# Kernel tuning notes

Hardware: AMD Instinct MI355X
Metric: run time of the kernel (lower is better)

## Reference

```python
import jax, jax.numpy as jnp
import numpy as np

B, N, D = 16, 2048, 1024
H, DH = 8, 64
I = H * DH            # 512
L = 64                # num_latents
DEPTH = 6
FF = 4 * D


def setup_inputs() -> dict:
    key = jax.random.key(0)
    ks = jax.random.split(key, 8)
    s = 0.02  # weight scale to keep activations well-conditioned
    return {
        "x": jax.random.normal(ks[0], (B, N, D), jnp.float32),
        "mask": jax.random.randint(ks[1], (B, N), 0, 2, jnp.int32),
        "latents": jax.random.normal(ks[2], (L, D), jnp.float32),
        "ln_m_w": jnp.ones((DEPTH, D), jnp.float32),
        "ln_m_b": jnp.zeros((DEPTH, D), jnp.float32),
        "ln_l_w": jnp.ones((DEPTH, D), jnp.float32),
        "ln_l_b": jnp.zeros((DEPTH, D), jnp.float32),
        "Wq": jax.random.normal(ks[3], (DEPTH, D, I), jnp.float32) * s,
        "Wkv": jax.random.normal(ks[4], (DEPTH, D, 2 * I), jnp.float32) * s,
        "Wo": jax.random.normal(ks[5], (DEPTH, I, D), jnp.float32) * s,
        "ff_ln_w": jnp.ones((DEPTH, D), jnp.float32),
        "ff_ln_b": jnp.zeros((DEPTH, D), jnp.float32),
        "W1": jax.random.normal(ks[6], (DEPTH, D, FF), jnp.float32) * s,
        "W2": jax.random.normal(ks[7], (DEPTH, FF, D), jnp.float32) * s,
        "norm_w": jnp.ones((D,), jnp.float32),
        "norm_b": jnp.zeros((D,), jnp.float32),
    }


def _ln(x, w, b, eps=1e-5):
    mu = x.mean(-1, keepdims=True)
    var = ((x - mu) ** 2).mean(-1, keepdims=True)
    return (x - mu) * jax.lax.rsqrt(var + eps) * w + b


def reference(x, mask, latents, ln_m_w, ln_m_b, ln_l_w, ln_l_b,
              Wq, Wkv, Wo, ff_ln_w, ff_ln_b, W1, W2, norm_w, norm_b):
    b, n, d = x.shape
    Lq = latents.shape[0]
    depth = Wq.shape[0]
    h = H
    dh = Wq.shape[-1] // h
    scale = dh ** -0.5

    x4 = x[:, None]  # b 1 n d  (t = 1 media frame)
    lat = jnp.broadcast_to(latents, (b, 1, Lq, d)).astype(x.dtype)
    # mask==1 means masked-out; latents (L zeros) are always attendable
    fmask = jnp.concatenate([mask, jnp.zeros((b, Lq), mask.dtype)], axis=-1)
    mbool = (fmask == 1)[:, None, None, None, :]  # b 1 1 1 S -> broadcast to b t h i S

    for i in range(depth):
        xn = _ln(x4, ln_m_w[i], ln_m_b[i])
        lnl = _ln(lat, ln_l_w[i], ln_l_b[i])
        q = (lnl @ Wq[i]).reshape(b, 1, Lq, h, dh)
        kv = jnp.concatenate([xn, lnl], axis=-2) @ Wkv[i]  # b 1 S 2I
        k, v = jnp.split(kv, 2, axis=-1)
        S = k.shape[-2]
        k = k.reshape(b, 1, S, h, dh)
        v = v.reshape(b, 1, S, h, dh)
        sim = jnp.einsum('btihd,btjhd->bthij', q, k) * scale
        sim = jnp.where(mbool, -jnp.inf, sim)
        sim = sim - jax.lax.stop_gradient(sim.max(axis=-1, keepdims=True))
        attn = jax.nn.softmax(sim, axis=-1)
        out = jnp.einsum('bthij,btjhd->btihd', attn, v).reshape(b, 1, Lq, h * dh)
        lat = out @ Wo[i] + lat
        hf = jax.nn.gelu(_ln(lat, ff_ln_w[i], ff_ln_b[i]) @ W1[i], approximate=False)
        lat = hf @ W2[i] + lat
    return _ln(lat, norm_w, norm_b)
```

## Files before the change

kernel.cpp:

```cpp
#include <hip/hip_runtime.h>

typedef unsigned short u16;
typedef unsigned int u32;
typedef __attribute__((ext_vector_type(8))) short short8;
typedef __attribute__((ext_vector_type(4))) float f4;

#define DEV static __device__ __forceinline__

constexpr int BB = 16, NN = 2048, DD = 1024, HH = 8, DHD = 64, II = 512, LL = 64, DEPTHC = 6, FFC = 4096;

DEV u16 f2bf(float f) {
  union { float f; u32 u; } v; v.f = f;
  u32 r = v.u + 0x7FFFu + ((v.u >> 16) & 1u);
  return (u16)(r >> 16);
}

DEV u32 pack2(float lo, float hi) {
  return (u32)f2bf(lo) | ((u32)f2bf(hi) << 16);
}

typedef const u32 __attribute__((address_space(1)))* gas_p;
typedef u32 __attribute__((address_space(3)))* las_p;
DEV void gl_lds16(const void* g, void* l) {
  __builtin_amdgcn_global_load_lds((gas_p)g, (las_p)l, 16, 0, 0);
}

__global__ __launch_bounds__(256) void maskscan_k(const int* __restrict__ mask,
    int* __restrict__ idx, int* __restrict__ cnt) {
  int b = blockIdx.x, tid = threadIdx.x;
  int lane = tid & 63, wv = tid >> 6;
  const int* mrow = mask + (size_t)b * NN;
  int base = tid * 8;
  int keep[8]; int local = 0;
  #pragma unroll
  for (int j = 0; j < 8; j++) { keep[j] = (mrow[base + j] == 0); local += keep[j]; }
  int incl = local;
  #pragma unroll
  for (int off = 1; off < 64; off <<= 1) {
    int v = __shfl_up(incl, off, 64);
    if (lane >= off) incl += v;
  }
  __shared__ int wsum[4];
  if (lane == 63) wsum[wv] = incl;
  __syncthreads();
  int wbase = 0;
  for (int w = 0; w < wv; w++) wbase += wsum[w];
  int pos = wbase + incl - local;
  #pragma unroll
  for (int j = 0; j < 8; j++) if (keep[j]) idx[(size_t)b * NN + pos++] = base + j;
  if (tid == 255) cnt[b] = wbase + incl;
}

__global__ void zero_k(float* __restrict__ p, int n) {
  int i = blockIdx.x * 256 + threadIdx.x;
  if (i < n) p[i] = 0.f;
}

__global__ __launch_bounds__(256) void transp_w_k(const float* __restrict__ Wa, u16* __restrict__ WTa,
    int R, int C, int ctLog) {
  __shared__ float t[64][65];
  int gid = blockIdx.x;
  int depth = gid >> 10;
  int l = gid & 1023;
  int c0 = (l & ((1 << ctLog) - 1)) << 6;
  int r0 = (l >> ctLog) << 6;
  const float* in = Wa + (size_t)depth * 4096 * 1024;
  u16* o1 = WTa + (size_t)depth * 4096 * 1024;
  int tid = threadIdx.x;
  int lr = tid >> 4, lc4 = (tid & 15) * 4;
  #pragma unroll
  for (int p = 0; p < 4; p++) {
    int row = p * 16 + lr;
    float4 v = *(const float4*)&in[(size_t)(r0 + row) * C + c0 + lc4];
    t[row][lc4] = v.x; t[row][lc4+1] = v.y; t[row][lc4+2] = v.z; t[row][lc4+3] = v.w;
  }
  __syncthreads();
  int oc = tid >> 3;
  int rg = tid & 7;
  #pragma unroll
  for (int p = 0; p < 2; p++) {
    int c = p * 32 + oc;
    float v[8];
    #pragma unroll
    for (int k = 0; k < 8; k++) v[k] = t[rg * 8 + k][c];
    int4 o;
    o.x = (int)pack2(v[0], v[1]); o.y = (int)pack2(v[2], v[3]);
    o.z = (int)pack2(v[4], v[5]); o.w = (int)pack2(v[6], v[7]);
    *(int4*)&o1[(size_t)(c0 + c) * R + r0 + rg * 8] = o;
  }
}

__global__ __launch_bounds__(256) void qkvo_fused_k(
    const float* __restrict__ WqA, const float* __restrict__ WkvA, const float* __restrict__ WoA,
    const float* __restrict__ lnwA, const float* __restrict__ lnbA,
    u16* __restrict__ WqkvTA, u16* __restrict__ WoTA, u16* __restrict__ WkvTfA,
    float* __restrict__ biaskvA,
    const float* __restrict__ x, const int* __restrict__ idx, const int* __restrict__ cnt,
    u16* __restrict__ xcomp, const float* __restrict__ latents, float* __restrict__ lat) {
  __shared__ float t[64][65];
  __shared__ float red8[8];
  int gid = blockIdx.x;
  int tid = threadIdx.x;
  if (gid < 3072) {
    int depth = gid >> 9;
    int id = gid & 511;
    const float* in; u16* o1; int R, C, c0, r0;
    bool iskv = false;
    if (id < 128)      { in = WqA  + (size_t)depth*1024*512;  R = 1024; C = 512;  int l = id;       c0 = (l & 7) * 64;  r0 = (l >> 3) * 64; o1 = WqkvTA + (size_t)depth*1536*1024; }
    else if (id < 384) { in = WkvA + (size_t)depth*1024*1024; R = 1024; C = 1024; int l = id - 128; c0 = (l & 15) * 64; r0 = (l >> 4) * 64; o1 = WqkvTA + (size_t)depth*1536*1024 + 512*1024; iskv = true; }
    else               { in = WoA  + (size_t)depth*512*1024;  R = 512;  C = 1024; int l = id - 384; c0 = (l & 15) * 64; r0 = (l >> 4) * 64; o1 = WoTA + (size_t)depth*1024*512; }
    int lr = tid >> 4, lc4 = (tid & 15) * 4;
    #pragma unroll
    for (int p = 0; p < 4; p++) {
      int row = p * 16 + lr;
      float4 v = *(const float4*)&in[(size_t)(r0 + row) * C + c0 + lc4];
      t[row][lc4] = v.x; t[row][lc4+1] = v.y; t[row][lc4+2] = v.z; t[row][lc4+3] = v.w;
    }
    int oc = tid >> 3;
    int rg = tid & 7;
    float lw[8], lb[8];
    if (iskv) {
      const float* lnw = lnwA + depth * 1024;
      const float* lnb = lnbA + depth * 1024;
      int rbase = r0 + rg * 8;
      float4 w0 = *(const float4*)&lnw[rbase];
      float4 w1 = *(const float4*)&lnw[rbase + 4];
      float4 b0 = *(const float4*)&lnb[rbase];
      float4 b1 = *(const float4*)&lnb[rbase + 4];
      lw[0]=w0.x; lw[1]=w0.y; lw[2]=w0.z; lw[3]=w0.w; lw[4]=w1.x; lw[5]=w1.y; lw[6]=w1.z; lw[7]=w1.w;
      lb[0]=b0.x; lb[1]=b0.y; lb[2]=b0.z; lb[3]=b0.w; lb[4]=b1.x; lb[5]=b1.y; lb[6]=b1.z; lb[7]=b1.w;
    }
    __syncthreads();
    #pragma unroll
    for (int p = 0; p < 2; p++) {
      int c = p * 32 + oc;
      float v[8];
      #pragma unroll
      for (int k = 0; k < 8; k++) v[k] = t[rg * 8 + k][c];
      int4 o;
      o.x = (int)pack2(v[0], v[1]); o.y = (int)pack2(v[2], v[3]);
      o.z = (int)pack2(v[4], v[5]); o.w = (int)pack2(v[6], v[7]);
      *(int4*)&o1[(size_t)(c0 + c) * R + r0 + rg * 8] = o;
      if (iskv) {
        u16* WkvTf = WkvTfA + (size_t)depth*1024*1024;
        int4 of;
        of.x = (int)pack2(v[0]*lw[0], v[1]*lw[1]); of.y = (int)pack2(v[2]*lw[2], v[3]*lw[3]);
        of.z = (int)pack2(v[4]*lw[4], v[5]*lw[5]); of.w = (int)pack2(v[6]*lw[6], v[7]*lw[7]);
        *(int4*)&WkvTf[(size_t)(c0 + c) * 1024 + r0 + rg * 8] = of;
        float partial = 0.f;
        #pragma unroll
        for (int k = 0; k < 8; k++) partial += lb[k] * v[k];
        partial += __shfl_xor(partial, 1, 64);
        partial += __shfl_xor(partial, 2, 64);
        partial += __shfl_xor(partial, 4, 64);
        if (rg == 0) atomicAdd(&biaskvA[depth*1024 + c0 + c], partial);
      }
    }
    return;
  }
  gid -= 3072;
  if (gid < 32768) {
    int b = gid >> 11, j = gid & 2047;
    int c = cnt[b];
    if (j >= ((c + 127) & ~127)) return;
    ushort4* orow = (ushort4*)(xcomp + ((size_t)b * NN + j) * DD);
    if (j >= c) { orow[tid] = make_ushort4(0, 0, 0, 0); return; }
    int src = idx[(size_t)b * NN + j];
    const float4* rp = (const float4*)(x + ((size_t)b * NN + src) * DD);
    float4 v = rp[tid];
    float s = v.x + v.y + v.z + v.w;
    float s2 = v.x*v.x + v.y*v.y + v.z*v.z + v.w*v.w;
    #pragma unroll
    for (int off = 32; off >= 1; off >>= 1) {
      s  += __shfl_xor(s, off, 64);
      s2 += __shfl_xor(s2, off, 64);
    }
    int wv = tid >> 6;
    if ((tid & 63) == 0) { red8[wv] = s; red8[4 + wv] = s2; }
    __syncthreads();
    s  = red8[0] + red8[1] + red8[2] + red8[3];
    s2 = red8[4] + red8[5] + red8[6] + red8[7];
    float mu = s * (1.f / DD);
    float var = s2 * (1.f / DD) - mu * mu;
    float rstd = rsqrtf(var + 1e-5f);
    orow[tid] = make_ushort4(f2bf((v.x - mu) * rstd), f2bf((v.y - mu) * rstd),
                             f2bf((v.z - mu) * rstd), f2bf((v.w - mu) * rstd));
    return;
  }
  gid -= 32768;
  int i2 = gid * 256 + tid;
  ((float4*)lat)[i2] = ((const float4*)latents)[i2 & (LL * DD / 4 - 1)];
}

template<bool OUTF32>
__global__ __launch_bounds__(256) void ln_rows_k(const float* __restrict__ in,
    const float* __restrict__ w, const float* __restrict__ bias, void* __restrict__ out) {
  int row = blockIdx.x;
  int tid = threadIdx.x;
  const float4* rp = (const float4*)(in + (size_t)row * DD);
  float4 x = rp[tid];
  float s = x.x + x.y + x.z + x.w;
  float s2 = x.x*x.x + x.y*x.y + x.z*x.z + x.w*x.w;
  #pragma unroll
  for (int off = 32; off >= 1; off >>= 1) {
    s  += __shfl_xor(s, off, 64);
    s2 += __shfl_xor(s2, off, 64);
  }
  __shared__ float red[8];
  int wv = tid >> 6;
  if ((tid & 63) == 0) { red[wv] = s; red[4 + wv] = s2; }
  __syncthreads();
  s  = red[0] + red[1] + red[2] + red[3];
  s2 = red[4] + red[5] + red[6] + red[7];
  float mu = s * (1.f / DD);
  float var = s2 * (1.f / DD) - mu * mu;
  float rstd = rsqrtf(var + 1e-5f);
  float y[4] = {x.x, x.y, x.z, x.w};
  int col = tid * 4;
  #pragma unroll
  for (int j = 0; j < 4; j++)
    y[j] = (y[j] - mu) * rstd * w[col + j] + bias[col + j];
  if (OUTF32) {
    float4 o = {y[0], y[1], y[2], y[3]};
    ((float4*)out)[(size_t)row * (DD/4) + tid] = o;
  } else {
    ushort4 o = make_ushort4(f2bf(y[0]), f2bf(y[1]), f2bf(y[2]), f2bf(y[3]));
    ((ushort4*)out)[(size_t)row * (DD/4) + tid] = o;
  }
}

__global__ __launch_bounds__(256) void gemm_fused_k(
    const u16* __restrict__ xcomp, const u16* __restrict__ WkvTf,
    u16* __restrict__ kvk, u16* __restrict__ vT,
    const float* __restrict__ bias, const int* __restrict__ cnt,
    const u16* __restrict__ lnl, const u16* __restrict__ WqkvT, u16* __restrict__ qkv) {
  __shared__ __align__(16) u16 As[128 * 32];
  __shared__ __align__(16) u16 Bs[128 * 32];
  int id = blockIdx.x;
  int tid = threadIdx.x;
  int wv = tid >> 6, lane = tid & 63;
  const u16 *A, *B;
  int m0, n0, batch = 0, ml = 0;
  bool iskv;
  if (id < 2048) {
    int xg = id & 7, t = id >> 3;
    int mtile = xg * 32 + (t >> 3);
    n0 = (t & 7) * 128;
    batch = mtile >> 4;
    ml = (mtile & 15) * 128;
    if (ml >= cnt[batch]) return;
    m0 = batch * NN + ml;
    A = xcomp; B = WkvTf; iskv = true;
  } else {
    int l = id - 2048;
    m0 = (l / 12) * 128; n0 = (l % 12) * 128;
    A = lnl; B = WqkvT; iskv = false;
  }
  const int K = 1024;
  int srow = wv * 16 + (lane >> 2);
  int scol = (lane & 3) * 8;
  const u16* gA0 = A + (size_t)(m0 + srow) * K + scol;
  const u16* gA1 = A + (size_t)(m0 + 64 + srow) * K + scol;
  const u16* gB0 = B + (size_t)(n0 + srow) * K + scol;
  const u16* gB1 = B + (size_t)(n0 + 64 + srow) * K + scol;
  u16* lA0 = &As[srow * 32 + scol];
  u16* lA1 = &As[(64 + srow) * 32 + scol];
  u16* lB0 = &Bs[srow * 32 + scol];
  u16* lB1 = &Bs[(64 + srow) * 32 + scol];
  int wm = (wv & 1) * 64, wn = (wv >> 1) * 64;
  int fr = lane & 15, fq = (lane >> 4) * 8;
  f4 acc[4][4];
  #pragma unroll
  for (int mi = 0; mi < 4; mi++)
    #pragma unroll
    for (int ni = 0; ni < 4; ni++) acc[mi][ni] = f4{0.f, 0.f, 0.f, 0.f};

  for (int k0 = 0; k0 < K; k0 += 32) {
    gl_lds16(gA0 + k0, lA0);
    gl_lds16(gA1 + k0, lA1);
    gl_lds16(gB0 + k0, lB0);
    gl_lds16(gB1 + k0, lB1);
    __syncthreads();
    short8 af[4], bfr[4];
    #pragma unroll
    for (int mi = 0; mi < 4; mi++)
      af[mi] = *(const short8*)&As[(wm + mi*16 + fr) * 32 + fq];
    #pragma unroll
    for (int ni = 0; ni < 4; ni++)
      bfr[ni] = *(const short8*)&Bs[(wn + ni*16 + fr) * 32 + fq];
    #pragma unroll
    for (int mi = 0; mi < 4; mi++)
      #pragma unroll
      for (int ni = 0; ni < 4; ni++)
        acc[mi][ni] = __builtin_amdgcn_mfma_f32_16x16x32_bf16(af[mi], bfr[ni], acc[mi][ni], 0, 0, 0);
    __syncthreads();
  }
  int er = (lane >> 4) * 4;
  int ec = lane & 15;
  if (iskv) {
    #pragma unroll
    for (int mi = 0; mi < 4; mi++) {
      int rbase = wm + mi*16 + er;
      #pragma unroll
      for (int ni = 0; ni < 4; ni++) {
        int col = n0 + wn + ni*16 + ec;
        float bv = bias[col];
        if (col < 512) {
          #pragma unroll
          for (int r = 0; r < 4; r++)
            kvk[(size_t)(m0 + rbase + r) * 512 + col] = f2bf(acc[mi][ni][r] + bv);
        } else {
          int d = col - 512;
          int hh = d >> 6, dl = d & 63;
          ushort4 o4;
          o4.x = f2bf(acc[mi][ni][0] + bv);
          o4.y = f2bf(acc[mi][ni][1] + bv);
          o4.z = f2bf(acc[mi][ni][2] + bv);
          o4.w = f2bf(acc[mi][ni][3] + bv);
          *(ushort4*)(vT + ((size_t)((batch * 8 + hh) * 64 + dl)) * NN + (ml + rbase)) = o4;
        }
      }
    }
  } else {
    #pragma unroll
    for (int mi = 0; mi < 4; mi++)
      #pragma unroll
      for (int ni = 0; ni < 4; ni++) {
        int col = n0 + wn + ni*16 + ec;
        #pragma unroll
        for (int r = 0; r < 4; r++) {
          int row = m0 + wm + mi*16 + er + r;
          qkv[(size_t)row * 1536 + col] = f2bf(acc[mi][ni][r]);
        }
      }
  }
}

__global__ __launch_bounds__(256) void gemm_gelu_k(const u16* __restrict__ A, const u16* __restrict__ Bm,
    u16* __restrict__ C, int M, int N, int K) {
  __shared__ __align__(16) u16 As[128 * 32];
  __shared__ __align__(16) u16 Bs[64 * 32];
  int tid = threadIdx.x;
  int wv = tid >> 6, lane = tid & 63;
  int m0 = blockIdx.y * 128, n0 = blockIdx.x * 64;
  int srow = wv * 16 + (lane >> 2);
  int scol = (lane & 3) * 8;
  const u16* gA0 = A + (size_t)(m0 + srow) * K + scol;
  const u16* gA1 = A + (size_t)(m0 + 64 + srow) * K + scol;
  const u16* gB0 = Bm + (size_t)(n0 + srow) * K + scol;
  u16* lA0 = &As[srow * 32 + scol];
  u16* lA1 = &As[(64 + srow) * 32 + scol];
  u16* lB0 = &Bs[srow * 32 + scol];
  int wm = (wv & 1) * 64, wn = (wv >> 1) * 32;
  int fr = lane & 15, fq = (lane >> 4) * 8;
  f4 acc[4][2];
  #pragma unroll
  for (int mi = 0; mi < 4; mi++)
    #pragma unroll
    for (int ni = 0; ni < 2; ni++) acc[mi][ni] = f4{0.f, 0.f, 0.f, 0.f};

  for (int k0 = 0; k0 < K; k0 += 32) {
    gl_lds16(gA0 + k0, lA0);
    gl_lds16(gA1 + k0, lA1);
    gl_lds16(gB0 + k0, lB0);
    __syncthreads();
    short8 af[4], bfr[2];
    #pragma unroll
    for (int mi = 0; mi < 4; mi++)
      af[mi] = *(const short8*)&As[(wm + mi*16 + fr) * 32 + fq];
    #pragma unroll
    for (int ni = 0; ni < 2; ni++)
      bfr[ni] = *(const short8*)&Bs[(wn + ni*16 + fr) * 32 + fq];
    #pragma unroll
    for (int mi = 0; mi < 4; mi++)
      #pragma unroll
      for (int ni = 0; ni < 2; ni++)
        acc[mi][ni] = __builtin_amdgcn_mfma_f32_16x16x32_bf16(af[mi], bfr[ni], acc[mi][ni], 0, 0, 0);
    __syncthreads();
  }
  int er = (lane >> 4) * 4;
  int ec = lane & 15;
  #pragma unroll
  for (int mi = 0; mi < 4; mi++)
    #pragma unroll
    for (int ni = 0; ni < 2; ni++) {
      int col = n0 + wn + ni*16 + ec;
      #pragma unroll
      for (int r = 0; r < 4; r++) {
        int row = m0 + wm + mi*16 + er + r;
        float v = acc[mi][ni][r];
        v = 0.5f * v * (1.f + erff(v * 0.70710678118654752f));
        C[(size_t)row * N + col] = f2bf(v);
      }
    }
}

__global__ __launch_bounds__(256) void gemmsk_k(const u16* __restrict__ A, const u16* __restrict__ Bm,
    float* __restrict__ C, int M, int N, int K, int Kc) {
  __shared__ __align__(16) u16 As[128 * 32];
  __shared__ __align__(16) u16 Bs[64 * 32];
  int tid = threadIdx.x;
  int wv = tid >> 6, lane = tid & 63;
  int m0 = blockIdx.y * 128, n0 = blockIdx.x * 64;
  int kb = blockIdx.z * Kc;
  int srow = wv * 16 + (lane >> 2);
  int scol = (lane & 3) * 8;
  const u16* gA0 = A + (size_t)(m0 + srow) * K + kb + scol;
  const u16* gA1 = A + (size_t)(m0 + 64 + srow) * K + kb + scol;
  const u16* gB0 = Bm + (size_t)(n0 + srow) * K + kb + scol;
  u16* lA0 = &As[srow * 32 + scol];
  u16* lA1 = &As[(64 + srow) * 32 + scol];
  u16* lB0 = &Bs[srow * 32 + scol];
  int wm = (wv & 1) * 64, wn = (wv >> 1) * 32;
  int fr = lane & 15, fq = (lane >> 4) * 8;
  f4 acc[4][2];
  #pragma unroll
  for (int mi = 0; mi < 4; mi++)
    #pragma unroll
    for (int ni = 0; ni < 2; ni++) acc[mi][ni] = f4{0.f, 0.f, 0.f, 0.f};

  for (int k0 = 0; k0 < Kc; k0 += 32) {
    gl_lds16(gA0 + k0, lA0);
    gl_lds16(gA1 + k0, lA1);
    gl_lds16(gB0 + k0, lB0);
    __syncthreads();
    short8 af[4], bfr[2];
    #pragma unroll
    for (int mi = 0; mi < 4; mi++)
      af[mi] = *(const short8*)&As[(wm + mi*16 + fr) * 32 + fq];
    #pragma unroll
    for (int ni = 0; ni < 2; ni++)
      bfr[ni] = *(const short8*)&Bs[(wn + ni*16 + fr) * 32 + fq];
    #pragma unroll
    for (int mi = 0; mi < 4; mi++)
      #pragma unroll
      for (int ni = 0; ni < 2; ni++)
        acc[mi][ni] = __builtin_amdgcn_mfma_f32_16x16x32_bf16(af[mi], bfr[ni], acc[mi][ni], 0, 0, 0);
    __syncthreads();
  }
  int er = (lane >> 4) * 4;
  int ec = lane & 15;
  #pragma unroll
  for (int mi = 0; mi < 4; mi++)
    #pragma unroll
    for (int ni = 0; ni < 2; ni++) {
      int col = n0 + wn + ni*16 + ec;
      #pragma unroll
      for (int r = 0; r < 4; r++) {
        int row = m0 + wm + mi*16 + er + r;
        atomicAdd(&C[(size_t)row * N + col], acc[mi][ni][r]);
      }
    }
}

__global__ __launch_bounds__(256) void attn_part_k(const u16* __restrict__ qkv,
    const u16* __restrict__ kvk, const u16* __restrict__ vT, const int* __restrict__ cnt,
    float* __restrict__ opart, float* __restrict__ mlpart) {
  int id = blockIdx.x;
  int b = id >> 5;
  int h = (id >> 2) & 7;
  int part = id & 3;
  int tid = threadIdx.x;
  int wv = tid >> 6, lane = tid & 63;
  int fr = lane & 15, fq8 = (lane >> 4) * 8;
  int c = cnt[b];
  int nt = (c + 63) >> 6;
  int T = nt + 1;
  int t0 = (T * part) >> 2;
  int t1 = (T * (part + 1)) >> 2;

  __shared__ __align__(16) u16 ks[64 * 88];
  __shared__ __align__(16) u16 vs[64 * 88];
  __shared__ __align__(16) u16 ps[4][16 * 88];
  __shared__ float smask[64];

  const u16* qp = qkv + (size_t)(b * LL + wv * 16 + fr) * 1536 + h * DHD;
  short8 aq0 = *(const short8*)(qp + fq8);
  short8 aq1 = *(const short8*)(qp + 32 + fq8);

  float m_i[4], l_i[4];
  f4 o[4];
  #pragma unroll
  for (int r = 0; r < 4; r++) { m_i[r] = -1e30f; l_i[r] = 0.f; }
  #pragma unroll
  for (int dt = 0; dt < 4; dt++) o[dt] = f4{0.f, 0.f, 0.f, 0.f};

  const float scale = 0.125f;

  for (int t = t0; t < t1; t++) {
    bool isLat = (t == nt);
    __syncthreads();
    if (isLat) {
      const u16* src = qkv + (size_t)(b * LL) * 1536 + 512 + h * DHD;
      #pragma unroll
      for (int it = 0; it < 2; it++) {
        int cid = it * 256 + tid;
        int kr = cid >> 3, c8 = (cid & 7) * 8;
        int4 kvv = *(const int4*)(src + (size_t)kr * 1536 + c8);
        *(int4*)&ks[kr * 88 + c8] = kvv;
        int4 vvv = *(const int4*)(src + 512 + (size_t)kr * 1536 + c8);
        const u16* ve = (const u16*)&vvv;
        #pragma unroll
        for (int j = 0; j < 8; j++) vs[(c8 + j) * 88 + kr] = ve[j];
      }
    } else {
      const u16* ksrc = kvk + (size_t)(b * NN + t * 64) * 512 + h * DHD;
      const u16* vsrc = vT + (size_t)((b * 8 + h) * 64) * NN + t * 64;
      #pragma unroll
      for (int it = 0; it < 2; it++) {
        int cid = it * 256 + tid;
        int kr = cid >> 3, c8 = (cid & 7) * 8;
        *(int4*)&ks[kr * 88 + c8] = *(const int4*)(ksrc + (size_t)kr * 512 + c8);
        *(int4*)&vs[kr * 88 + c8] = *(const int4*)(vsrc + (size_t)kr * NN + c8);
      }
    }
    if (tid < 64)
      smask[tid] = (isLat || (t * 64 + tid < c)) ? 0.f : -1e30f;
    __syncthreads();

    f4 sim[4];
    #pragma unroll
    for (int ct = 0; ct < 4; ct++) {
      short8 b0 = *(const short8*)&ks[(ct*16 + fr) * 88 + fq8];
      short8 b1 = *(const short8*)&ks[(ct*16 + fr) * 88 + 32 + fq8];
      f4 s = f4{0.f, 0.f, 0.f, 0.f};
      s = __builtin_amdgcn_mfma_f32_16x16x32_bf16(aq0, b0, s, 0, 0, 0);
      s = __builtin_amdgcn_mfma_f32_16x16x32_bf16(aq1, b1, s, 0, 0, 0);
      float mk = smask[ct*16 + fr];
      #pragma unroll
      for (int r = 0; r < 4; r++) s[r] = s[r] * scale + mk;
      sim[ct] = s;
    }
    float mnew[4], alpha[4], p[4][4];
    #pragma unroll
    for (int r = 0; r < 4; r++) {
      float mx = fmaxf(fmaxf(sim[0][r], sim[1][r]), fmaxf(sim[2][r], sim[3][r]));
      #pragma unroll
      for (int off = 8; off >= 1; off >>= 1) mx = fmaxf(mx, __shfl_xor(mx, off, 16));
      mnew[r] = fmaxf(m_i[r], mx);
      alpha[r] = __expf(m_i[r] - mnew[r]);
      m_i[r] = mnew[r];
      float ssum = 0.f;
      #pragma unroll
      for (int ct = 0; ct < 4; ct++) { float e = __expf(sim[ct][r] - mnew[r]); p[ct][r] = e; ssum += e; }
      #pragma unroll
      for (int off = 8; off >= 1; off >>= 1) ssum += __shfl_xor(ssum, off, 16);
      l_i[r] = l_i[r] * alpha[r] + ssum;
    }
    #pragma unroll
    for (int ct = 0; ct < 4; ct++)
      #pragma unroll
      for (int r = 0; r < 4; r++)
        ps[wv][((lane>>4)*4 + r) * 88 + ct*16 + fr] = f2bf(p[ct][r]);
    #pragma unroll
    for (int dt = 0; dt < 4; dt++)
      #pragma unroll
      for (int r = 0; r < 4; r++) o[dt][r] *= alpha[r];
    short8 pa0 = *(const short8*)&ps[wv][fr * 88 + fq8];
    short8 pa1 = *(const short8*)&ps[wv][fr * 88 + 32 + fq8];
    #pragma unroll
    for (int dt = 0; dt < 4; dt++) {
      short8 bv0 = *(const short8*)&vs[(dt*16 + fr) * 88 + fq8];
      short8 bv1 = *(const short8*)&vs[(dt*16 + fr) * 88 + 32 + fq8];
      o[dt] = __builtin_amdgcn_mfma_f32_16x16x32_bf16(pa0, bv0, o[dt], 0, 0, 0);
      o[dt] = __builtin_amdgcn_mfma_f32_16x16x32_bf16(pa1, bv1, o[dt], 0, 0, 0);
    }
  }
  #pragma unroll
  for (int dt = 0; dt < 4; dt++)
    #pragma unroll
    for (int r = 0; r < 4; r++) {
      int row = wv * 16 + (lane>>4)*4 + r;
      int col = dt*16 + fr;
      opart[((size_t)id * 64 + row) * 64 + col] = o[dt][r];
    }
  if (fr == 0) {
    #pragma unroll
    for (int r = 0; r < 4; r++) {
      int row = wv * 16 + (lane>>4)*4 + r;
      mlpart[id * 128 + row * 2]     = m_i[r];
      mlpart[id * 128 + row * 2 + 1] = l_i[r];
    }
  }
}

__global__ __launch_bounds__(256) void attn_comb_k(const float* __restrict__ opart,
    const float* __restrict__ mlpart, u16* __restrict__ out) {
  int bh = blockIdx.x;
  int b = bh >> 3, h = bh & 7;
  int tid = threadIdx.x;
  int row = tid >> 2;
  int c0 = (tid & 3) * 16;
  float mp[4], lp[4];
  float m = -1e30f;
  #pragma unroll
  for (int p = 0; p < 4; p++) {
    mp[p] = mlpart[(bh * 4 + p) * 128 + row * 2];
    lp[p] = mlpart[(bh * 4 + p) * 128 + row * 2 + 1];
    m = fmaxf(m, mp[p]);
  }
  float a[4]; float L = 0.f;
  #pragma unroll
  for (int p = 0; p < 4; p++) { a[p] = __expf(mp[p] - m); L += lp[p] * a[p]; }
  float rl = 1.f / L;
  u16* op = out + ((size_t)(b * LL + row)) * II + h * DHD + c0;
  #pragma unroll
  for (int j = 0; j < 4; j++) {
    float acc4[4] = {0.f, 0.f, 0.f, 0.f};
    #pragma unroll
    for (int p = 0; p < 4; p++) {
      const float4* pp = (const float4*)(opart + ((size_t)(bh * 4 + p) * 64 + row) * 64 + c0);
      float4 v = pp[j];
      acc4[0] += v.x * a[p]; acc4[1] += v.y * a[p];
      acc4[2] += v.z * a[p]; acc4[3] += v.w * a[p];
    }
    op[j*4 + 0] = f2bf(acc4[0] * rl);
    op[j*4 + 1] = f2bf(acc4[1] * rl);
    op[j*4 + 2] = f2bf(acc4[2] * rl);
    op[j*4 + 3] = f2bf(acc4[3] * rl);
  }
}

extern "C" void kernel_launch(void* const* d_in, const int* in_sizes, int n_in,
                              void* d_out, int out_size, void* d_ws, size_t ws_size,
                              hipStream_t stream) {
  (void)in_sizes; (void)n_in; (void)out_size; (void)ws_size;
  const float* x       = (const float*)d_in[0];
  const int*   mask    = (const int*)d_in[1];
  const float* latents = (const float*)d_in[2];
  const float* ln_m_w  = (const float*)d_in[3];
  const float* ln_m_b  = (const float*)d_in[4];
  const float* ln_l_w  = (const float*)d_in[5];
  const float* ln_l_b  = (const float*)d_in[6];
  const float* Wq      = (const float*)d_in[7];
  const float* Wkv     = (const float*)d_in[8];
  const float* Wo      = (const float*)d_in[9];
  const float* ff_ln_w = (const float*)d_in[10];
  const float* ff_ln_b = (const float*)d_in[11];
  const float* W1      = (const float*)d_in[12];
  const float* W2      = (const float*)d_in[13];
  const float* norm_w  = (const float*)d_in[14];
  const float* norm_b  = (const float*)d_in[15];
  float* out = (float*)d_out;

  char* ws = (char*)d_ws;
  size_t off = 0;
  auto alloc = [&](size_t bytes) -> void* {
    void* p = ws + off; off += (bytes + 255) & ~(size_t)255; return p;
  };
  u16* xcomp = (u16*)alloc((size_t)32768 * 1024 * 2);
  u16* kvk   = (u16*)alloc((size_t)32768 * 512 * 2);
  u16* vT    = (u16*)alloc((size_t)8192 * 2048 * 2);
  int* idxb  = (int*)alloc((size_t)32768 * 4);
  int* cnt   = (int*)alloc(64);
  float* lat = (float*)alloc((size_t)1024 * 1024 * 4);
  u16* lnl   = (u16*)alloc((size_t)1024 * 1024 * 2);
  u16* latn  = (u16*)alloc((size_t)1024 * 1024 * 2);
  u16* qkv   = (u16*)alloc((size_t)1024 * 1536 * 2);
  u16* aout  = (u16*)alloc((size_t)1024 * 512 * 2);
  u16* hf    = (u16*)alloc((size_t)1024 * 4096 * 2);
  float* opart  = (float*)alloc((size_t)512 * 64 * 64 * 4);
  float* mlpart = (float*)alloc((size_t)512 * 128 * 4);
  u16* WqkvT = (u16*)alloc((size_t)DEPTHC * 1536 * 1024 * 2);
  u16* WkvTf = (u16*)alloc((size_t)DEPTHC * 1024 * 1024 * 2);
  u16* WoT   = (u16*)alloc((size_t)DEPTHC * 1024 * 512 * 2);
  u16* W1T   = (u16*)alloc((size_t)DEPTHC * 4096 * 1024 * 2);
  u16* W2T   = (u16*)alloc((size_t)DEPTHC * 1024 * 4096 * 2);
  float* biaskv_all = (float*)alloc(DEPTHC * 1024 * 4);

  maskscan_k<<<16, 256, 0, stream>>>(mask, idxb, cnt);
  zero_k<<<24, 256, 0, stream>>>(biaskv_all, DEPTHC * 1024);
  transp_w_k<<<DEPTHC * 1024, 256, 0, stream>>>(W1, W1T, 1024, 4096, 6);
  transp_w_k<<<DEPTHC * 1024, 256, 0, stream>>>(W2, W2T, 4096, 1024, 4);
  qkvo_fused_k<<<3072 + 32768 + 1024, 256, 0, stream>>>(
      Wq, Wkv, Wo, ln_m_w, ln_m_b,
      WqkvT, WoT, WkvTf, biaskv_all,
      x, idxb, cnt, xcomp, latents, lat);

  for (int i = 0; i < DEPTHC; i++) {
    ln_rows_k<false><<<1024, 256, 0, stream>>>(lat, ln_l_w + i*1024, ln_l_b + i*1024, lnl);
    gemm_fused_k<<<2144, 256, 0, stream>>>(
        xcomp, WkvTf + (size_t)i*1024*1024, kvk, vT, biaskv_all + i*1024, cnt,
        lnl, WqkvT + (size_t)i*1536*1024, qkv);
    attn_part_k<<<512, 256, 0, stream>>>(qkv, kvk, vT, cnt, opart, mlpart);
    attn_comb_k<<<128, 256, 0, stream>>>(opart, mlpart, aout);
    gemmsk_k<<<dim3(16, 8, 4), 256, 0, stream>>>(aout, WoT + (size_t)i*1024*512, lat, 1024, 1024, 512, 128);
    ln_rows_k<false><<<1024, 256, 0, stream>>>(lat, ff_ln_w + i*1024, ff_ln_b + i*1024, latn);
    gemm_gelu_k<<<dim3(64, 8), 256, 0, stream>>>(latn, W1T + (size_t)i*4096*1024, hf, 1024, 4096, 1024);
    gemmsk_k<<<dim3(16, 8, 4), 256, 0, stream>>>(hf, W2T + (size_t)i*1024*4096, lat, 1024, 1024, 4096, 1024);
  }
  ln_rows_k<true><<<1024, 256, 0, stream>>>(lat, norm_w, norm_b, out);
}
```

Measured before the change: 1.459 ms.

## Enlarge fused KV/QKV GEMM tile to 256x128 with k-chunked LDS layout

The fused KV/Q GEMM now uses 256x128 output tiles in place of 128x128. Each wave computes 128x64 with 8x4 MFMA accumulators, which halves the block count and raises operand reuse per LDS load. The LDS layout changes to k-chunk-major (8-element chunks by row) so each thread loads one full A row slice, and launch bounds request 2 blocks per SM. Compacted x rows are now zero-padded to a multiple of 256 to match the tile. The risks are more register pressure from 128 accumulator floats, more wasted work on partially valid tiles, and fewer blocks for load balance.

```diff
diff --git a/kernel.cpp b/kernel.cpp
--- a/kernel.cpp
+++ b/kernel.cpp
@@ -162,7 +162,7 @@
   if (gid < 32768) {
     int b = gid >> 11, j = gid & 2047;
     int c = cnt[b];
-    if (j >= ((c + 127) & ~127)) return;
+    if (j >= ((c + 255) & ~255)) return;
     ushort4* orow = (ushort4*)(xcomp + ((size_t)b * NN + j) * DD);
     if (j >= c) { orow[tid] = make_ushort4(0, 0, 0, 0); return; }
     int src = idx[(size_t)b * NN + j];
@@ -229,67 +229,65 @@
   }
 }
 
-__global__ __launch_bounds__(256) void gemm_fused_k(
+__global__ __launch_bounds__(256, 2) void gemm_fused_k(
     const u16* __restrict__ xcomp, const u16* __restrict__ WkvTf,
     u16* __restrict__ kvk, u16* __restrict__ vT,
     const float* __restrict__ bias, const int* __restrict__ cnt,
     const u16* __restrict__ lnl, const u16* __restrict__ WqkvT, u16* __restrict__ qkv) {
-  __shared__ __align__(16) u16 As[128 * 32];
-  __shared__ __align__(16) u16 Bs[128 * 32];
+  __shared__ __align__(16) u16 As[4 * 256 * 8];
+  __shared__ __align__(16) u16 Bs[4 * 128 * 8];
   int id = blockIdx.x;
   int tid = threadIdx.x;
   int wv = tid >> 6, lane = tid & 63;
   const u16 *A, *B;
   int m0, n0, batch = 0, ml = 0;
   bool iskv;
-  if (id < 2048) {
+  if (id < 1024) {
     int xg = id & 7, t = id >> 3;
-    int mtile = xg * 32 + (t >> 3);
+    int mtile = xg * 16 + (t >> 3);
     n0 = (t & 7) * 128;
-    batch = mtile >> 4;
-    ml = (mtile & 15) * 128;
+    batch = mtile >> 3;
+    ml = (mtile & 7) * 256;
     if (ml >= cnt[batch]) return;
     m0 = batch * NN + ml;
     A = xcomp; B = WkvTf; iskv = true;
   } else {
-    int l = id - 2048;
-    m0 = (l / 12) * 128; n0 = (l % 12) * 128;
+    int l = id - 1024;
+    m0 = (l / 12) * 256; n0 = (l % 12) * 128;
     A = lnl; B = WqkvT; iskv = false;
   }
   const int K = 1024;
-  int srow = wv * 16 + (lane >> 2);
-  int scol = (lane & 3) * 8;
-  const u16* gA0 = A + (size_t)(m0 + srow) * K + scol;
-  const u16* gA1 = A + (size_t)(m0 + 64 + srow) * K + scol;
-  const u16* gB0 = B + (size_t)(n0 + srow) * K + scol;
-  const u16* gB1 = B + (size_t)(n0 + 64 + srow) * K + scol;
-  u16* lA0 = &As[srow * 32 + scol];
-  u16* lA1 = &As[(64 + srow) * 32 + scol];
-  u16* lB0 = &Bs[srow * 32 + scol];
-  u16* lB1 = &Bs[(64 + srow) * 32 + scol];
-  int wm = (wv & 1) * 64, wn = (wv >> 1) * 64;
+  const u16* gA = A + (size_t)(m0 + tid) * K;
+  const u16* gB = B + (size_t)(n0 + (tid & 127)) * K + (tid >> 7) * 8;
+  u16* lA = &As[tid * 8];
+  u16* lB = &Bs[(tid >> 7) * 1024 + (tid & 127) * 8];
+  int wr = wv >> 1, wc = wv & 1;
   int fr = lane & 15, fq = (lane >> 4) * 8;
-  f4 acc[4][4];
-  #pragma unroll
-  for (int mi = 0; mi < 4; mi++)
+  int arow0 = wr * 128 + fr;
+  int brow0 = wc * 64 + fr;
+  f4 acc[8][4];
+  #pragma unroll
+  for (int mi = 0; mi < 8; mi++)
     #pragma unroll
     for (int ni = 0; ni < 4; ni++) acc[mi][ni] = f4{0.f, 0.f, 0.f, 0.f};
 
   for (int k0 = 0; k0 < K; k0 += 32) {
-    gl_lds16(gA0 + k0, lA0);
-    gl_lds16(gA1 + k0, lA1);
-    gl_lds16(gB0 + k0, lB0);
-    gl_lds16(gB1 + k0, lB1);
-    __syncthreads();
-    short8 af[4], bfr[4];
-    #pragma unroll
-    for (int mi = 0; mi < 4; mi++)
-      af[mi] = *(const short8*)&As[(wm + mi*16 + fr) * 32 + fq];
+    #pragma unroll
+    for (int c = 0; c < 4; c++)
+      gl_lds16(gA + k0 + c * 8, lA + c * 2048);
+    #pragma unroll
+    for (int c = 0; c < 2; c++)
+      gl_lds16(gB + k0 + c * 16, lB + c * 2048);
+    __syncthreads();
+    short8 af[8], bfr[4];
+    #pragma unroll
+    for (int mi = 0; mi < 8; mi++)
+      af[mi] = *(const short8*)&As[fq * 256 + (arow0 + mi * 16) * 8];
     #pragma unroll
     for (int ni = 0; ni < 4; ni++)
-      bfr[ni] = *(const short8*)&Bs[(wn + ni*16 + fr) * 32 + fq];
-    #pragma unroll
-    for (int mi = 0; mi < 4; mi++)
+      bfr[ni] = *(const short8*)&Bs[fq * 128 + (brow0 + ni * 16) * 8];
+    #pragma unroll
+    for (int mi = 0; mi < 8; mi++)
       #pragma unroll
       for (int ni = 0; ni < 4; ni++)
         acc[mi][ni] = __builtin_amdgcn_mfma_f32_16x16x32_bf16(af[mi], bfr[ni], acc[mi][ni], 0, 0, 0);
@@ -299,11 +297,11 @@
   int ec = lane & 15;
   if (iskv) {
     #pragma unroll
-    for (int mi = 0; mi < 4; mi++) {
-      int rbase = wm + mi*16 + er;
+    for (int mi = 0; mi < 8; mi++) {
+      int rbase = wr * 128 + mi * 16 + er;
       #pragma unroll
       for (int ni = 0; ni < 4; ni++) {
-        int col = n0 + wn + ni*16 + ec;
+        int col = n0 + wc * 64 + ni * 16 + ec;
         float bv = bias[col];
         if (col < 512) {
           #pragma unroll
@@ -323,16 +321,16 @@
     }
   } else {
     #pragma unroll
-    for (int mi = 0; mi < 4; mi++)
+    for (int mi = 0; mi < 8; mi++) {
+      int rbase = wr * 128 + mi * 16 + er;
       #pragma unroll
       for (int ni = 0; ni < 4; ni++) {
-        int col = n0 + wn + ni*16 + ec;
+        int col = n0 + wc * 64 + ni * 16 + ec;
         #pragma unroll
-        for (int r = 0; r < 4; r++) {
-          int row = m0 + wm + mi*16 + er + r;
-          qkv[(size_t)row * 1536 + col] = f2bf(acc[mi][ni][r]);
-        }
+        for (int r = 0; r < 4; r++)
+          qkv[(size_t)(m0 + rbase + r) * 1536 + col] = f2bf(acc[mi][ni][r]);
       }
+    }
   }
 }
 
@@ -679,7 +677,7 @@
 
   for (int i = 0; i < DEPTHC; i++) {
     ln_rows_k<false><<<1024, 256, 0, stream>>>(lat, ln_l_w + i*1024, ln_l_b + i*1024, lnl);
-    gemm_fused_k<<<2144, 256, 0, stream>>>(
+    gemm_fused_k<<<1072, 256, 0, stream>>>(
         xcomp, WkvTf + (size_t)i*1024*1024, kvk, vT, biaskv_all + i*1024, cnt,
         lnl, WqkvT + (size_t)i*1536*1024, qkv);
     attn_part_k<<<512, 256, 0, stream>>>(qkv, kvk, vT, cnt, opart, mlpart);
```

Measured after the change: 1.670 ms. 1.14x slower.
